# Optimization experiments

Hardware: AMD Instinct MI355X
Metric: run time of the kernel (lower is better)

Reference implementation:

```python
import jax, jax.numpy as jnp
import numpy as np

B, S, HID = 1, 2048, 4096
H, KV, D = 32, 8, 128
SOFTCAP = 50.0
WINDOW = 1024
SCALE = 128 ** -0.5  # query_pre_attn_scalar = 128
NEG = -2.3819763e38
ROPE_BASE = 10000.0


def _rope(x, positions):
    # x: (B, S, h, D); positions: (S,) int
    d = x.shape[-1]
    inv_freq = 1.0 / (ROPE_BASE ** (jnp.arange(0, d, 2, dtype=jnp.float32) / d))
    phase = positions.astype(jnp.float32)[:, None] * inv_freq        # (S, D/2)
    phase = jnp.concatenate([phase, phase], axis=-1)[None, :, None, :]  # (1,S,1,D)
    x1, x2 = jnp.split(x, 2, axis=-1)
    rotated = jnp.concatenate([-x2, x1], axis=-1)
    return (x * jnp.cos(phase) + rotated * jnp.sin(phase)).astype(x.dtype)


def setup_inputs() -> dict:
    key = jax.random.key(0)
    k0, k1, k2 = jax.random.split(key, 3)
    hidden_states = jax.random.normal(k0, (B, S, HID), dtype=jnp.float32)
    kv_write_indices = jnp.arange(S, dtype=jnp.int32)
    k_cache = jnp.zeros((B, S, KV, D), dtype=jnp.float32)
    v_cache = jnp.zeros((B, S, KV, D), dtype=jnp.float32)
    # additive causal mask: 0 where j<=i, else large negative
    causal = jnp.tril(jnp.ones((S, S), dtype=bool))
    mask = jnp.where(causal, 0.0, NEG)[None, None].astype(jnp.float32)
    qkv_w = jax.random.normal(k1, (HID, (H + 2 * KV) * D), dtype=jnp.float32) * 0.02
    o_w = jax.random.normal(k2, (H * D, HID), dtype=jnp.float32) * 0.02
    return {"hidden_states": hidden_states, "kv_write_indices": kv_write_indices,
            "k_cache": k_cache, "v_cache": v_cache, "mask": mask,
            "qkv_w": qkv_w, "o_w": o_w}


def reference(hidden_states, kv_write_indices, k_cache, v_cache, mask, qkv_w, o_w):
    b, s, _ = hidden_states.shape
    qkv = hidden_states @ qkv_w                                   # (B,S,(H+2KV)*D)
    xq, xk, xv = jnp.split(qkv, [H * D, H * D + KV * D], axis=-1)
    xq = xq.reshape(b, s, H, D)
    xk = xk.reshape(b, s, KV, D)
    xv = xv.reshape(b, s, KV, D)
    xq = _rope(xq, kv_write_indices)
    xk = _rope(xk, kv_write_indices)
    # KV cache write (index_copy_ along seq dim)
    k_cache = k_cache.at[:, kv_write_indices].set(xk)
    v_cache = v_cache.at[:, kv_write_indices].set(xv)
    # GQA: repeat kv heads
    rep = H // KV
    key = jnp.repeat(k_cache, rep, axis=2)                        # (B,T,H,D)
    value = jnp.repeat(v_cache, rep, axis=2)
    q = jnp.transpose(xq, (0, 2, 1, 3)) * SCALE                   # (B,H,S,D)
    k = jnp.transpose(key, (0, 2, 1, 3))                          # (B,H,T,D)
    v = jnp.transpose(value, (0, 2, 1, 3))
    scores = jnp.einsum('bhqd,bhkd->bhqk', q, k)                  # (B,H,S,T)
    # sliding-window band mask: keep |i-j| <= WINDOW-1, else NEG
    t = k.shape[2]
    i = jnp.arange(s)[:, None]
    j = jnp.arange(t)[None, :]
    band = jnp.abs(i - j) <= (WINDOW - 1)
    mask = jnp.where(band[None, None], mask, NEG)
    # tanh softcapping
    scores = jnp.tanh(scores / SOFTCAP) * SOFTCAP
    scores = scores + mask
    probs = jax.nn.softmax(scores.astype(jnp.float32), axis=-1).astype(q.dtype)
    out = jnp.einsum('bhqk,bhkd->bhqd', probs, v)                 # (B,H,S,D)
    out = jnp.transpose(out, (0, 2, 1, 3)).reshape(b, s, H * D)
    return out @ o_w
```

## Files before the change

kernel.cpp:

```cpp
#include <hip/hip_runtime.h>
#include <hip/hip_bf16.h>
#include <cstdint>
#include <cstddef>

#define S_LEN   2048
#define HIDDEN  4096
#define NH      32
#define NKV     8
#define HD      128
#define NQKV    6144
#define WINDOW  1024
#define QSCALE  0.0883883476483184f
#define NEGBIG  -1e30f

typedef __attribute__((ext_vector_type(8))) short  short8;
typedef __attribute__((ext_vector_type(4))) float  f32x4;
typedef __attribute__((ext_vector_type(4))) unsigned short us4;

__device__ __forceinline__ unsigned short f2bf(float f) {
  union { float f; uint32_t u; } v; v.f = f;
  uint32_t r = v.u + 0x7FFFu + ((v.u >> 16) & 1u);
  return (unsigned short)(r >> 16);
}

__device__ __forceinline__ void gload_lds16(const void* g, void* l) {
  __builtin_amdgcn_global_load_lds(
      (const __attribute__((address_space(1))) unsigned int*)g,
      (__attribute__((address_space(3))) unsigned int*)l, 16, 0, 0);
}

__global__ __launch_bounds__(256) void cast_f32_bf16_kernel(
    const float* __restrict__ src, unsigned short* __restrict__ dst, int n4) {
  int i = blockIdx.x * 256 + threadIdx.x;
  if (i >= n4) return;
  float4 v = ((const float4*)src)[i];
  us4 o; o.x = f2bf(v.x); o.y = f2bf(v.y); o.z = f2bf(v.z); o.w = f2bf(v.w);
  ((us4*)dst)[i] = o;
}

__global__ __launch_bounds__(256) void transpose_cast_kernel(
    const float* __restrict__ src, unsigned short* __restrict__ dst,
    long srstride, long dstride, long szoff, long dzoff) {
  __shared__ float tile[32][33];
  src += (long)blockIdx.z * szoff;
  dst += (long)blockIdx.z * dzoff;
  const int c0 = blockIdx.x * 32, r0 = blockIdx.y * 32;
  const int tx = threadIdx.x, ty = threadIdx.y;
#pragma unroll
  for (int i = 0; i < 32; i += 8)
    tile[ty + i][tx] = src[(long)(r0 + ty + i) * srstride + c0 + tx];
  __syncthreads();
#pragma unroll
  for (int i = 0; i < 32; i += 8)
    dst[(long)(c0 + ty + i) * dstride + r0 + tx] = f2bf(tile[tx][ty + i]);
}

__global__ __launch_bounds__(256) void rope_table_kernel(float* __restrict__ T) {
  int idx = blockIdx.x * 256 + threadIdx.x;
  int pos = idx >> 6, f = idx & 63;
  float inv = powf(10000.0f, -(float)(2 * f) / 128.0f);
  float ang = (float)pos * inv;
  T[idx * 2 + 0] = cosf(ang);
  T[idx * 2 + 1] = sinf(ang);
}

__global__ __launch_bounds__(256) void rope_scatter_kernel(
    const float* __restrict__ qkv, const float* __restrict__ T,
    unsigned short* __restrict__ Qb, unsigned short* __restrict__ Kb) {
  const int s = blockIdx.x;
  const float* row = qkv + (long)s * NQKV;
  const float* tr  = T + (long)s * 128;
#pragma unroll
  for (int it = 0; it < 10; ++it) {
    int hp = it * 256 + threadIdx.x;
    int head = hp >> 6, dd = hp & 63;
    float c = tr[dd * 2], sn = tr[dd * 2 + 1];
    int srcoff = (head < NH) ? head * HD : HIDDEN + (head - NH) * HD;
    float x1 = row[srcoff + dd], x2 = row[srcoff + dd + 64];
    float o1 = x1 * c - x2 * sn;
    float o2 = x2 * c + x1 * sn;
    if (head < NH) {
      unsigned short* q = Qb + ((long)head * S_LEN + s) * HD;
      q[dd]      = f2bf(o1 * QSCALE);
      q[dd + 64] = f2bf(o2 * QSCALE);
    } else {
      unsigned short* k = Kb + ((long)(head - NH) * S_LEN + s) * HD;
      k[dd]      = f2bf(o1);
      k[dd + 64] = f2bf(o2);
    }
  }
}

__global__ __launch_bounds__(256) void gemm_bt_kernel(
    const unsigned short* __restrict__ A, const unsigned short* __restrict__ BT,
    float* __restrict__ C, int M, int N, int K) {
  __shared__ unsigned short As[128][32];
  __shared__ unsigned short Bs[128][32];
  const int tid  = threadIdx.x;
  const int lane = tid & 63, wave = tid >> 6;
  const int wm = wave >> 1, wn = wave & 1;
  const int r16 = lane & 15, g4 = lane >> 4;

  const int nwg  = gridDim.x * gridDim.y;
  const int orig = blockIdx.y * gridDim.x + blockIdx.x;
  const int cpx  = nwg >> 3;
  const int swz  = (orig & 7) * cpx + (orig >> 3);
  const long bm = (long)(swz / gridDim.x) * 128;
  const long bn = (long)(swz % gridDim.x) * 128;

  f32x4 acc[4][4] = {};

  const int s0 = tid, s1 = tid + 256;
  const int r0 = s0 >> 2, c0 = s0 & 3;
  const int r1 = s1 >> 2, c1 = s1 & 3;

  for (int k0 = 0; k0 < K; k0 += 32) {
    __syncthreads();
    gload_lds16(A  + (bm + r0) * K + k0 + c0 * 8, &As[0][0] + s0 * 8);
    gload_lds16(BT + (bn + r0) * K + k0 + c0 * 8, &Bs[0][0] + s0 * 8);
    gload_lds16(A  + (bm + r1) * K + k0 + c1 * 8, &As[0][0] + s1 * 8);
    gload_lds16(BT + (bn + r1) * K + k0 + c1 * 8, &Bs[0][0] + s1 * 8);
    __syncthreads();

    short8 a[4], b[4];
#pragma unroll
    for (int m = 0; m < 4; ++m)
      a[m] = *(const short8*)&As[wm * 64 + m * 16 + r16][g4 * 8];
#pragma unroll
    for (int n = 0; n < 4; ++n)
      b[n] = *(const short8*)&Bs[wn * 64 + n * 16 + r16][g4 * 8];
#pragma unroll
    for (int m = 0; m < 4; ++m)
#pragma unroll
      for (int n = 0; n < 4; ++n)
        acc[m][n] = __builtin_amdgcn_mfma_f32_16x16x32_bf16(a[m], b[n], acc[m][n], 0, 0, 0);
  }

  float* Cp = C + (bm + wm * 64) * N + bn + wn * 64;
#pragma unroll
  for (int m = 0; m < 4; ++m)
#pragma unroll
    for (int n = 0; n < 4; ++n)
#pragma unroll
      for (int r = 0; r < 4; ++r)
        Cp[(long)(m * 16 + g4 * 4 + r) * N + n * 16 + r16] = acc[m][n][r];
}

__global__ __launch_bounds__(256) void attn_kernel(
    const unsigned short* __restrict__ Qb, const unsigned short* __restrict__ Kb,
    const unsigned short* __restrict__ VT, unsigned short* __restrict__ attnB) {
  const int h  = blockIdx.y;
  const int qt = (blockIdx.x + blockIdx.y) & 31;
  const int q0 = qt * 64;
  const int kv = h >> 2;
  const int tid  = threadIdx.x;
  const int lane = tid & 63, wave = tid >> 6;
  const int r16 = lane & 15, g4 = lane >> 4;
  const int qrow = q0 + wave * 16;

  __shared__ unsigned short Ks[64 * 128];
  __shared__ unsigned short Vs[128 * 64];
  __shared__ unsigned short Pl[4][16][72];

  short8 qf[4];
  const unsigned short* Qrow = Qb + ((long)h * S_LEN + qrow + r16) * HD;
#pragma unroll
  for (int kk = 0; kk < 4; ++kk)
    qf[kk] = *(const short8*)(Qrow + kk * 32 + g4 * 8);

  float l_[4] = {0.f, 0.f, 0.f, 0.f};
  f32x4 Of[8] = {};

  const unsigned short* Kbase = Kb + (long)kv * S_LEN * HD;
  const unsigned short* Vbase = VT + (long)kv * HD * S_LEN;

  int jstart = q0 - (WINDOW - 1);
  jstart = (jstart < 0) ? 0 : (jstart & ~63);

  for (int j0 = jstart; j0 < q0 + 64; j0 += 64) {
    __syncthreads();
#pragma unroll
    for (int it = 0; it < 4; ++it) {
      int ci = it * 256 + tid;
      int r  = ci >> 4, c = ci & 15;
      int cl = c ^ (r & 7);
      gload_lds16(Kbase + (long)(j0 + r) * HD + cl * 8, Ks + ci * 8);
    }
#pragma unroll
    for (int it = 0; it < 4; ++it) {
      int ci = it * 256 + tid;
      int r  = ci >> 3, c = ci & 7;
      int cl = c ^ (r & 7);
      gload_lds16(Vbase + (long)r * S_LEN + j0 + cl * 8, Vs + ci * 8);
    }
    __syncthreads();

    f32x4 sf[4] = {};
#pragma unroll
    for (int kk = 0; kk < 4; ++kk) {
#pragma unroll
      for (int n = 0; n < 4; ++n) {
        short8 kf = *(const short8*)(Ks + (n * 16 + r16) * 128 +
                                     ((kk * 4 + g4) ^ (r16 & 7)) * 8);
        sf[n] = __builtin_amdgcn_mfma_f32_16x16x32_bf16(qf[kk], kf, sf[n], 0, 0, 0);
      }
    }
#pragma unroll
    for (int n = 0; n < 4; ++n) {
      int j = j0 + n * 16 + r16;
#pragma unroll
      for (int r = 0; r < 4; ++r) {
        int i = qrow + g4 * 4 + r;
        float v = sf[n][r];
        float e = __expf(v * 0.04f);
        float cap = 50.0f - 100.0f * __builtin_amdgcn_rcpf(e + 1.0f);
        bool ok = (j <= i) && (j >= i - (WINDOW - 1));
        float p = ok ? __expf(cap) : 0.0f;
        l_[r] += p;
        Pl[wave][g4 * 4 + r][n * 16 + r16] = f2bf(p);
      }
    }
#pragma unroll
    for (int ks = 0; ks < 2; ++ks) {
      short8 af = *(const short8*)&Pl[wave][r16][ks * 32 + g4 * 8];
#pragma unroll
      for (int n = 0; n < 8; ++n) {
        short8 vf = *(const short8*)(Vs + (n * 16 + r16) * 64 +
                                     ((ks * 4 + g4) ^ (r16 & 7)) * 8);
        Of[n] = __builtin_amdgcn_mfma_f32_16x16x32_bf16(af, vf, Of[n], 0, 0, 0);
      }
    }
  }
#pragma unroll
  for (int r = 0; r < 4; ++r) {
#pragma unroll
    for (int off = 1; off < 16; off <<= 1)
      l_[r] += __shfl_xor(l_[r], off, 64);
    l_[r] = __builtin_amdgcn_rcpf(l_[r]);
  }
#pragma unroll
  for (int n = 0; n < 8; ++n)
#pragma unroll
    for (int r = 0; r < 4; ++r) {
      int i = qrow + g4 * 4 + r;
      float o = Of[n][r] * l_[r];
      attnB[(long)i * (NH * HD) + h * HD + n * 16 + r16] = f2bf(o);
    }
}

extern "C" void kernel_launch(void* const* d_in, const int* in_sizes, int n_in,
                              void* d_out, int out_size, void* d_ws, size_t ws_size,
                              hipStream_t stream) {
  const float* hidden = (const float*)d_in[0];
  const float* qkv_w  = (const float*)d_in[5];
  const float* o_w    = (const float*)d_in[6];
  float* out = (float*)d_out;
  char* ws = (char*)d_ws;

  unsigned short* hidB  = (unsigned short*)(ws);
  unsigned short* wqkvT = (unsigned short*)(ws + 16777216L);
  unsigned short* woT   = (unsigned short*)(ws + 67108864L);
  float*          qkvF  = (float*)        (ws + 100663296L);
  unsigned short* Qb    = (unsigned short*)(ws + 150994944L);
  unsigned short* Kb    = (unsigned short*)(ws + 167772160L);
  unsigned short* VT    = (unsigned short*)(ws + 171966464L);
  unsigned short* attnB = (unsigned short*)(ws + 176160768L);
  float*          ropeT = (float*)        (ws + 192937984L);

  cast_f32_bf16_kernel<<<(S_LEN * HIDDEN / 4 + 255) / 256, 256, 0, stream>>>(
      hidden, hidB, S_LEN * HIDDEN / 4);
  transpose_cast_kernel<<<dim3(NQKV / 32, HIDDEN / 32, 1), dim3(32, 8), 0, stream>>>(
      qkv_w, wqkvT, NQKV, HIDDEN, 0, 0);
  transpose_cast_kernel<<<dim3(HIDDEN / 32, NH * HD / 32, 1), dim3(32, 8), 0, stream>>>(
      o_w, woT, HIDDEN, NH * HD, 0, 0);
  rope_table_kernel<<<(S_LEN * 64) / 256, 256, 0, stream>>>(ropeT);
  gemm_bt_kernel<<<dim3(NQKV / 128, S_LEN / 128), 256, 0, stream>>>(
      hidB, wqkvT, qkvF, S_LEN, NQKV, HIDDEN);
  rope_scatter_kernel<<<S_LEN, 256, 0, stream>>>(qkvF, ropeT, Qb, Kb);
  transpose_cast_kernel<<<dim3(HD / 32, S_LEN / 32, NKV), dim3(32, 8), 0, stream>>>(
      qkvF + HIDDEN + NKV * HD, VT, NQKV, S_LEN, HD, (long)HD * S_LEN);
  attn_kernel<<<dim3(S_LEN / 64, NH), 256, 0, stream>>>(Qb, Kb, VT, attnB);
  gemm_bt_kernel<<<dim3(NH * HD / 128, S_LEN / 128), 256, 0, stream>>>(
      attnB, woT, out, S_LEN, NH * HD, HIDDEN);
}
```

Measured before the change: 619.7 us.

## Replace GEMM with 8-wave double-buffered, swizzled-LDS large-tile kernel

Replaces the 128x128, 4-wave, single-buffered GEMM with an 8-wave kernel using 256xBN tiles, K-step 64, and a double-buffered LDS pipeline. The next tile's global-to-LDS loads are issued before the MFMAs run, so memory latency overlaps with compute. LDS columns are XOR-swizzled to avoid bank conflicts, and setprio/barriers are added around the MFMA bursts. The larger tiles raise register use and LDS footprint, and with BN=256 the QKV GEMM launches only 192 workgroups, which may underfill the GPU.

```diff
diff --git a/kernel.cpp b/kernel.cpp
--- a/kernel.cpp
+++ b/kernel.cpp
@@ -91,56 +91,87 @@
   }
 }
 
-__global__ __launch_bounds__(256) void gemm_bt_kernel(
+template<int BN>
+__global__ __launch_bounds__(512, 2) void gemm8p_kernel(
     const unsigned short* __restrict__ A, const unsigned short* __restrict__ BT,
     float* __restrict__ C, int M, int N, int K) {
-  __shared__ unsigned short As[128][32];
-  __shared__ unsigned short Bs[128][32];
+  constexpr int WN  = BN / 4;
+  constexpr int NFR = WN / 16;
+  constexpr int ASZ = 256 * 64;
+  constexpr int BSZ = BN * 64;
+
+  __shared__ unsigned short lds[2 * (ASZ + BSZ)];
+
   const int tid  = threadIdx.x;
   const int lane = tid & 63, wave = tid >> 6;
-  const int wm = wave >> 1, wn = wave & 1;
+  const int wm = wave >> 2, wn = wave & 3;
   const int r16 = lane & 15, g4 = lane >> 4;
 
   const int nwg  = gridDim.x * gridDim.y;
   const int orig = blockIdx.y * gridDim.x + blockIdx.x;
-  const int cpx  = nwg >> 3;
-  const int swz  = (orig & 7) * cpx + (orig >> 3);
-  const long bm = (long)(swz / gridDim.x) * 128;
-  const long bn = (long)(swz % gridDim.x) * 128;
-
-  f32x4 acc[4][4] = {};
-
-  const int s0 = tid, s1 = tid + 256;
-  const int r0 = s0 >> 2, c0 = s0 & 3;
-  const int r1 = s1 >> 2, c1 = s1 & 3;
-
-  for (int k0 = 0; k0 < K; k0 += 32) {
+  const int swz  = (orig & 7) * (nwg >> 3) + (orig >> 3);
+  const long bm = (long)(swz / gridDim.x) * 256;
+  const long bn = (long)(swz % gridDim.x) * BN;
+
+  f32x4 acc[8][NFR] = {};
+
+  auto STAGE = [&](int k0, int buf) {
+    unsigned short* la = lds + buf * (ASZ + BSZ);
+    unsigned short* lb = la + ASZ;
+#pragma unroll
+    for (int j = 0; j < 4; ++j) {
+      int ci = tid + j * 512;
+      int row = ci >> 3, cl = (ci & 7) ^ (row & 7);
+      gload_lds16(A + (bm + row) * K + k0 + cl * 8, la + ci * 8);
+    }
+#pragma unroll
+    for (int j = 0; j < BN / 64; ++j) {
+      int ci = tid + j * 512;
+      int row = ci >> 3, cl = (ci & 7) ^ (row & 7);
+      gload_lds16(BT + (bn + row) * K + k0 + cl * 8, lb + ci * 8);
+    }
+  };
+
+  const int NT = K >> 6;
+  STAGE(0, 0);
+  __syncthreads();
+
+  for (int t = 0; t < NT; ++t) {
+    const int cur = t & 1;
+    const unsigned short* la = lds + cur * (ASZ + BSZ);
+    const unsigned short* lb = la + ASZ;
+    if (t + 1 < NT) STAGE((t + 1) << 6, cur ^ 1);
+#pragma unroll
+    for (int kk = 0; kk < 2; ++kk) {
+      short8 af[8], bf[NFR];
+#pragma unroll
+      for (int m = 0; m < 8; ++m) {
+        int row = wm * 128 + m * 16 + r16;
+        af[m] = *(const short8*)(la + row * 64 + (((kk << 2) | g4) ^ (r16 & 7)) * 8);
+      }
+#pragma unroll
+      for (int n = 0; n < NFR; ++n) {
+        int row = wn * WN + n * 16 + r16;
+        bf[n] = *(const short8*)(lb + row * 64 + (((kk << 2) | g4) ^ (r16 & 7)) * 8);
+      }
+      __builtin_amdgcn_s_barrier();
+      __builtin_amdgcn_s_setprio(1);
+#pragma unroll
+      for (int m = 0; m < 8; ++m)
+#pragma unroll
+        for (int n = 0; n < NFR; ++n)
+          acc[m][n] = __builtin_amdgcn_mfma_f32_16x16x32_bf16(af[m], bf[n], acc[m][n], 0, 0, 0);
+      __builtin_amdgcn_s_setprio(0);
+      if (kk == 0) __builtin_amdgcn_s_barrier();
+    }
     __syncthreads();
-    gload_lds16(A  + (bm + r0) * K + k0 + c0 * 8, &As[0][0] + s0 * 8);
-    gload_lds16(BT + (bn + r0) * K + k0 + c0 * 8, &Bs[0][0] + s0 * 8);
-    gload_lds16(A  + (bm + r1) * K + k0 + c1 * 8, &As[0][0] + s1 * 8);
-    gload_lds16(BT + (bn + r1) * K + k0 + c1 * 8, &Bs[0][0] + s1 * 8);
-    __syncthreads();
-
-    short8 a[4], b[4];
-#pragma unroll
-    for (int m = 0; m < 4; ++m)
-      a[m] = *(const short8*)&As[wm * 64 + m * 16 + r16][g4 * 8];
-#pragma unroll
-    for (int n = 0; n < 4; ++n)
-      b[n] = *(const short8*)&Bs[wn * 64 + n * 16 + r16][g4 * 8];
-#pragma unroll
-    for (int m = 0; m < 4; ++m)
-#pragma unroll
-      for (int n = 0; n < 4; ++n)
-        acc[m][n] = __builtin_amdgcn_mfma_f32_16x16x32_bf16(a[m], b[n], acc[m][n], 0, 0, 0);
   }
 
-  float* Cp = C + (bm + wm * 64) * N + bn + wn * 64;
-#pragma unroll
-  for (int m = 0; m < 4; ++m)
-#pragma unroll
-    for (int n = 0; n < 4; ++n)
+  float* Cp = C + (bm + wm * 128) * N + bn + wn * WN;
+#pragma unroll
+  for (int m = 0; m < 8; ++m)
+#pragma unroll
+    for (int n = 0; n < NFR; ++n)
 #pragma unroll
       for (int r = 0; r < 4; ++r)
         Cp[(long)(m * 16 + g4 * 4 + r) * N + n * 16 + r16] = acc[m][n][r];
@@ -274,12 +305,12 @@
   transpose_cast_kernel<<<dim3(HIDDEN / 32, NH * HD / 32, 1), dim3(32, 8), 0, stream>>>(
       o_w, woT, HIDDEN, NH * HD, 0, 0);
   rope_table_kernel<<<(S_LEN * 64) / 256, 256, 0, stream>>>(ropeT);
-  gemm_bt_kernel<<<dim3(NQKV / 128, S_LEN / 128), 256, 0, stream>>>(
+  gemm8p_kernel<256><<<dim3(NQKV / 256, S_LEN / 256), 512, 0, stream>>>(
       hidB, wqkvT, qkvF, S_LEN, NQKV, HIDDEN);
   rope_scatter_kernel<<<S_LEN, 256, 0, stream>>>(qkvF, ropeT, Qb, Kb);
   transpose_cast_kernel<<<dim3(HD / 32, S_LEN / 32, NKV), dim3(32, 8), 0, stream>>>(
       qkvF + HIDDEN + NKV * HD, VT, NQKV, S_LEN, HD, (long)HD * S_LEN);
   attn_kernel<<<dim3(S_LEN / 64, NH), 256, 0, stream>>>(Qb, Kb, VT, attnB);
-  gemm_bt_kernel<<<dim3(NH * HD / 128, S_LEN / 128), 256, 0, stream>>>(
+  gemm8p_kernel<128><<<dim3(NH * HD / 128, S_LEN / 256), 512, 0, stream>>>(
       attnB, woT, out, S_LEN, NH * HD, HIDDEN);
 }
```

Result: faster. 563.8 us (-9.0%).
